# Performance work log

Measured on AMD Instinct MI355X. Metric: run time of the kernel, lower is better.

The kernel has to match this reference:

```python
import jax, jax.numpy as jnp
import numpy as np

B, M, IN, H = 4096, 16, 512, 512


def _linear_params(key, out_dim, in_dim):
    kw, kb = jax.random.split(key)
    s = 1.0 / np.sqrt(in_dim)
    W = jax.random.uniform(kw, (out_dim, in_dim), jnp.float32, -s, s)
    b = jax.random.uniform(kb, (out_dim,), jnp.float32, -s, s)
    return W, b


def setup_inputs() -> dict:
    key = jax.random.key(0)
    ks = jax.random.split(key, 15)
    inp = {
        "input": jax.random.normal(ks[0], (B, IN), jnp.float32),
        "h0": jax.random.normal(ks[1], (B, H), jnp.float32),
        "c0": jax.random.normal(ks[2], (B, H), jnp.float32),
        "all_c_b_e_w": jax.random.normal(ks[3], (B, M, H), jnp.float32),
        "all_num_word": jax.random.randint(ks[4], (B,), 0, M + 1, jnp.int32),
    }
    names = ["ii", "hi", "if_", "hf", "ig", "hg", "io", "ho", "lx", "lc"]
    in_dims = [IN, H, IN, H, IN, H, IN, H, IN, H]
    for n, d, k in zip(names, in_dims, ks[5:15]):
        W, b = _linear_params(k, H, d)
        inp["W_" + n] = W
        inp["b_" + n] = b
    return inp


def _lin(x, W, b):
    return x @ W.T + b


def reference(input, h0, c0, all_c_b_e_w, all_num_word,
              W_ii, b_ii, W_hi, b_hi, W_if_, b_if_, W_hf, b_hf,
              W_ig, b_ig, W_hg, b_hg, W_io, b_io, W_ho, b_ho,
              W_lx, b_lx, W_lc, b_lc):
    i = jax.nn.sigmoid(_lin(input, W_ii, b_ii) + _lin(h0, W_hi, b_hi))   # [B,H]
    f = jax.nn.sigmoid(_lin(input, W_if_, b_if_) + _lin(h0, W_hf, b_hf))  # computed but unused, as in original
    g = jnp.tanh(_lin(input, W_ig, b_ig) + _lin(h0, W_hg, b_hg))         # [B,H]
    o = jax.nn.sigmoid(_lin(input, W_io, b_io) + _lin(h0, W_ho, b_ho))   # [B,H]

    # lattice word-cell gates, vectorized over the ragged word dim with a mask
    lx = _lin(input, W_lx, b_lx)                 # [B,H]
    lc = _lin(all_c_b_e_w, W_lc, b_lc)           # [B,M,H]
    i_b = jax.nn.sigmoid(lx[:, None, :] + lc)    # [B,M,H]
    mask = (jnp.arange(M)[None, :] < all_num_word[:, None])  # [B,M]
    exp_b = jnp.exp(i_b) * mask[:, :, None].astype(i_b.dtype)  # [B,M,H]
    exp_i = jnp.exp(i)                                         # [B,H]
    denom = exp_i + jnp.sum(exp_b, axis=1)                     # [B,H]
    c_words = jnp.sum((exp_b / denom[:, None, :]) * all_c_b_e_w, axis=1)
    c_lat = c_words + (exp_i / denom) * g
    c = jnp.where((all_num_word > 0)[:, None], c_lat, g)       # num_word==0 -> c=g
    h1 = o * jnp.tanh(c)
    return (h1, c)
```

## Files before the change

### kernel.cpp

```cpp
#include <hip/hip_runtime.h>
#include <hip/hip_bf16.h>
#include <stdint.h>


typedef __attribute__((ext_vector_type(8))) short short8;
typedef __attribute__((ext_vector_type(4))) float f32x4;
typedef __attribute__((ext_vector_type(4))) unsigned short us4;

__device__ __forceinline__ unsigned short f2bf(float f) {
  union { float f; unsigned u; } v; v.f = f;
  return (unsigned short)((v.u + 0x7fffu + ((v.u >> 16) & 1u)) >> 16);
}
__device__ __forceinline__ unsigned short f2bf_h(float f) {
  __hip_bfloat16 h = __float2bfloat16(f);
  return *reinterpret_cast<unsigned short*>(&h);
}
__device__ __forceinline__ float bf2f(unsigned short u) {
  return __uint_as_float((unsigned)u << 16);
}
__device__ __forceinline__ float sigmoidf_(float x) {
  return 1.f / (1.f + __expf(-x));
}
__device__ __forceinline__ float fast_tanh(float x) {
  float e = __expf(-2.f * fmaxf(x, -30.f));
  return (1.f - e) / (1.f + e);
}

__global__ void k_cvt_all(const float* __restrict__ x, const float* __restrict__ h,
                          const float* __restrict__ Wii, const float* __restrict__ Wig,
                          const float* __restrict__ Wio, const float* __restrict__ Wlx,
                          const float* __restrict__ Whi, const float* __restrict__ Whg,
                          const float* __restrict__ Who, const float* __restrict__ Wlcf,
                          unsigned short* __restrict__ XH, unsigned short* __restrict__ Wcat,
                          unsigned short* __restrict__ Wlc) {
  const int bb = blockIdx.x;
  const int tid = threadIdx.x;
  us4 o;
  if (bb < 4096) {
    const int t = bb * 256 + tid;
    const int b = t >> 8;
    const int col = (t & 255) * 4;
    const float* src = (col < 512) ? (x + (size_t)b * 512 + col)
                                   : (h + (size_t)b * 512 + (col - 512));
    f32x4 v = *(const f32x4*)src;
    o[0] = f2bf(v[0]); o[1] = f2bf(v[1]); o[2] = f2bf(v[2]); o[3] = f2bf(v[3]);
    *(us4*)(XH + (size_t)t * 4) = o;
  } else if (bb < 6144) {
    const int t = (bb - 4096) * 256 + tid;
    const int row = t >> 8;
    const int col = (t & 255) * 4;
    const int sec = row >> 9, r = row & 511;
    if (col < 512) {
      const float* W = sec == 0 ? Wii : sec == 1 ? Wig : sec == 2 ? Wio : Wlx;
      f32x4 v = *(const f32x4*)(W + (size_t)r * 512 + col);
      o[0] = f2bf(v[0]); o[1] = f2bf(v[1]); o[2] = f2bf(v[2]); o[3] = f2bf(v[3]);
    } else if (sec < 3) {
      const float* W = sec == 0 ? Whi : sec == 1 ? Whg : Who;
      f32x4 v = *(const f32x4*)(W + (size_t)r * 512 + (col - 512));
      o[0] = f2bf(v[0]); o[1] = f2bf(v[1]); o[2] = f2bf(v[2]); o[3] = f2bf(v[3]);
    } else {
      o[0] = 0; o[1] = 0; o[2] = 0; o[3] = 0;
    }
    *(us4*)(Wcat + (size_t)t * 4) = o;
  } else {
    const int t = (bb - 6144) * 256 + tid;
    f32x4 v = *(const f32x4*)(Wlcf + (size_t)t * 4);
    o[0] = f2bf(v[0]); o[1] = f2bf(v[1]); o[2] = f2bf(v[2]); o[3] = f2bf(v[3]);
    *(us4*)(Wlc + (size_t)t * 4) = o;
  }
}

__global__ __launch_bounds__(1024) void k_scan(const int* __restrict__ nwp,
                                               int* __restrict__ off,
                                               int* __restrict__ row_map) {
  const int tid = threadIdx.x;
  const int lane = tid & 63, wid = tid >> 6;
  __shared__ int wsum[16];
  __shared__ int stotal;
  int n[4];
  int s = 0;
#pragma unroll
  for (int i = 0; i < 4; ++i) {
    int v = nwp[tid * 4 + i];
    v = min(max(v, 0), 16);
    n[i] = v; s += v;
  }
  int sc = s;
  for (int d = 1; d < 64; d <<= 1) {
    int t = __shfl_up(sc, d, 64);
    if (lane >= d) sc += t;
  }
  if (lane == 63) wsum[wid] = sc;
  __syncthreads();
  if (tid == 0) {
    int acc = 0;
    for (int w = 0; w < 16; ++w) { int t = wsum[w]; wsum[w] = acc; acc += t; }
    stotal = acc;
  }
  __syncthreads();
  int excl = wsum[wid] + sc - s;
#pragma unroll
  for (int i = 0; i < 4; ++i) {
    const int b = tid * 4 + i;
    off[b] = excl;
    for (int m = 0; m < n[i]; ++m) row_map[excl + m] = b * 16 + m;
    excl += n[i];
  }
  __syncthreads();
  const int total = stotal;
  if (tid == 0) off[4096] = total;
  const int padded = (total + 255) & ~255;
  for (int idx = total + tid; idx < padded; idx += 1024) row_map[idx] = 0;
}

__global__ __launch_bounds__(256) void k_gemm0(
    const unsigned short* __restrict__ A, const unsigned short* __restrict__ Bm,
    unsigned short* __restrict__ C, int Ndim, int Kdim, int nbx) {
  __shared__ unsigned short As[2][128 * 64];
  __shared__ unsigned short Bs[2][128 * 64];
  const int tid = threadIdx.x;
  const int lane = tid & 63, wid = tid >> 6;
  const int wr = wid >> 1, wc = wid & 1;
  const int l15 = lane & 15, lhi = lane >> 4;

  const int chunk = gridDim.x >> 3;
  const int bid = (blockIdx.x & 7) * chunk + (blockIdx.x >> 3);
  const int brow = bid / nbx, bcol = bid % nbx;
  const int m0 = brow * 128, n0 = bcol * 128;

  f32x4 acc[4][4];
#pragma unroll
  for (int i = 0; i < 4; ++i)
#pragma unroll
    for (int j = 0; j < 4; ++j) acc[i][j] = (f32x4){0.f, 0.f, 0.f, 0.f};

  const int cb0 = wid * 64;
  auto stage = [&](int buf, int k0) {
#pragma unroll
    for (int q = 0; q < 4; ++q) {
      const int cb = q * 256 + cb0;
      const int chunkid = cb + lane;
      const int row = chunkid >> 3, slot = chunkid & 7;
      const int kk = k0 + ((slot ^ (row & 7)) << 3);
      __builtin_amdgcn_global_load_lds(
          (const __attribute__((address_space(1))) unsigned int*)(A + (size_t)(m0 + row) * Kdim + kk),
          (__attribute__((address_space(3))) unsigned int*)(As[buf] + cb * 8), 16, 0, 0);
      __builtin_amdgcn_global_load_lds(
          (const __attribute__((address_space(1))) unsigned int*)(Bm + (size_t)(n0 + row) * Kdim + kk),
          (__attribute__((address_space(3))) unsigned int*)(Bs[buf] + cb * 8), 16, 0, 0);
    }
  };

  const int nt = Kdim >> 6;
  stage(0, 0);
  __syncthreads();

  const int swz = (lane & 7) << 4;
  for (int t = 0; t < nt; ++t) {
    const int cur = t & 1;
    if (t + 1 < nt) stage(cur ^ 1, (t + 1) << 6);
    const char* Ab = (const char*)As[cur];
    const char* Bb = (const char*)Bs[cur];
#pragma unroll
    for (int s = 0; s < 2; ++s) {
      short8 av[4], bv[4];
#pragma unroll
      for (int mi = 0; mi < 4; ++mi) {
        const int row = wr * 64 + mi * 16 + l15;
        av[mi] = *(const short8*)(Ab + row * 128 + ((s * 64 + lhi * 16) ^ swz));
      }
#pragma unroll
      for (int ni = 0; ni < 4; ++ni) {
        const int row = wc * 64 + ni * 16 + l15;
        bv[ni] = *(const short8*)(Bb + row * 128 + ((s * 64 + lhi * 16) ^ swz));
      }
#pragma unroll
      for (int mi = 0; mi < 4; ++mi)
#pragma unroll
        for (int ni = 0; ni < 4; ++ni)
          acc[mi][ni] = __builtin_amdgcn_mfma_f32_16x16x32_bf16(av[mi], bv[ni], acc[mi][ni], 0, 0, 0);
    }
    __syncthreads();
  }

#pragma unroll
  for (int mi = 0; mi < 4; ++mi) {
    const int gr = m0 + wr * 64 + mi * 16 + lhi * 4;
#pragma unroll
    for (int ni = 0; ni < 4; ++ni) {
      const int gc = n0 + wc * 64 + ni * 16 + l15;
#pragma unroll
      for (int j = 0; j < 4; ++j)
        C[(size_t)(gr + j) * Ndim + gc] = f2bf(acc[mi][ni][j]);
    }
  }
}

__global__ __launch_bounds__(512) void k_latg(
    const float* __restrict__ Af,
    const unsigned short* __restrict__ Bm,
    const int* __restrict__ row_map,
    const int* __restrict__ totalp,
    unsigned short* __restrict__ lcb) {
  __shared__ unsigned short As[2][256 * 32];
  __shared__ unsigned short Bs[2][256 * 32];
  const int tid = threadIdx.x;
  const int lane = tid & 63, wid = tid >> 6;
  const int wrow = wid >> 2, wcol = wid & 3;
  const int l15 = lane & 15, lhi = lane >> 4;

  const int total = totalp[0];
  const int nact = ((total + 255) >> 8) << 1;
  const int chunk = gridDim.x >> 3;
  const int bid = (blockIdx.x & 7) * chunk + (blockIdx.x >> 3);
  if (bid >= nact) return;
  const int brow = bid >> 1, bcol = bid & 1;
  const int m0 = brow * 256, n0 = bcol * 256;

  int orow0 = row_map[m0 + (tid >> 2)];
  int orow1 = row_map[m0 + 128 + (tid >> 2)];

  f32x4 acc[8][4];
#pragma unroll
  for (int i = 0; i < 8; ++i)
#pragma unroll
    for (int j = 0; j < 4; ++j) acc[i][j] = (f32x4){0.f, 0.f, 0.f, 0.f};

  f32x4 SA[2][2], SB[2][2];

  auto loadA = [&](f32x4 (&dst)[2][2], int k0) {
#pragma unroll
    for (int q = 0; q < 2; ++q) {
      const int orow = q ? orow1 : orow0;
      const int s = tid & 3;
      const float* p = Af + (size_t)orow * 512 + k0 + s * 8;
      dst[q][0] = *(const f32x4*)p;
      dst[q][1] = *(const f32x4*)(p + 4);
    }
  };
  auto writeA = [&](int buf, f32x4 (&src)[2][2]) {
#pragma unroll
    for (int q = 0; q < 2; ++q) {
      const int c = q * 512 + tid;
      const int row = c >> 2, s = c & 3;
      const int pr = row >> 1;
      const int phys = (s + ((row & 1) << 2)) ^ (pr & 7);
      short8 v;
      v[0] = (short)f2bf_h(src[q][0][0]); v[1] = (short)f2bf_h(src[q][0][1]);
      v[2] = (short)f2bf_h(src[q][0][2]); v[3] = (short)f2bf_h(src[q][0][3]);
      v[4] = (short)f2bf_h(src[q][1][0]); v[5] = (short)f2bf_h(src[q][1][1]);
      v[6] = (short)f2bf_h(src[q][1][2]); v[7] = (short)f2bf_h(src[q][1][3]);
      *(short8*)((char*)As[buf] + pr * 128 + phys * 16) = v;
    }
  };
  auto stageB = [&](int buf, int k0) {
#pragma unroll
    for (int q = 0; q < 2; ++q) {
      const int cb = q * 512 + wid * 64;
      const int c = cb + lane;
      const int pr = c >> 3, phys = c & 7;
      const int gi = phys ^ (pr & 7);
      const int row = pr * 2 + (gi >> 2);
      const int kk = k0 + ((gi & 3) << 3);
      __builtin_amdgcn_global_load_lds(
          (const __attribute__((address_space(1))) unsigned int*)(Bm + (size_t)(n0 + row) * 512 + kk),
          (__attribute__((address_space(3))) unsigned int*)(Bs[buf] + cb * 8), 16, 0, 0);
    }
  };

  auto compute = [&](int buf) {
    const char* Ab = (const char*)As[buf];
    const char* Bb = (const char*)Bs[buf];
    short8 av[8], bv[4];
#pragma unroll
    for (int mi = 0; mi < 8; ++mi) {
      const int row = wrow * 128 + mi * 16 + l15;
      const int pr = row >> 1;
      av[mi] = *(const short8*)(Ab + pr * 128 +
                (((lhi + ((row & 1) << 2)) ^ (pr & 7)) << 4));
    }
#pragma unroll
    for (int ni = 0; ni < 4; ++ni) {
      const int row = wcol * 64 + ni * 16 + l15;
      const int pr = row >> 1;
      bv[ni] = *(const short8*)(Bb + pr * 128 +
                (((lhi + ((row & 1) << 2)) ^ (pr & 7)) << 4));
    }
    __builtin_amdgcn_s_setprio(1);
#pragma unroll
    for (int mi = 0; mi < 8; ++mi)
#pragma unroll
      for (int ni = 0; ni < 4; ++ni)
        acc[mi][ni] = __builtin_amdgcn_mfma_f32_16x16x32_bf16(av[mi], bv[ni], acc[mi][ni], 0, 0, 0);
    __builtin_amdgcn_s_setprio(0);
  };

  loadA(SA, 0);
  loadA(SB, 32);
  stageB(0, 0);
  writeA(0, SA);
  __syncthreads();

#pragma unroll 1
  for (int t = 0; t < 16; t += 2) {
    if (t + 2 < 16) loadA(SA, (t + 2) << 5);
    if (t + 1 < 16) stageB(1, (t + 1) << 5);
    compute(0);
    if (t + 1 < 16) writeA(1, SB);
    __syncthreads();
    if (t + 3 < 16) loadA(SB, (t + 3) << 5);
    if (t + 2 < 16) stageB(0, (t + 2) << 5);
    compute(1);
    if (t + 2 < 16) writeA(0, SA);
    __syncthreads();
  }

#pragma unroll
  for (int mi = 0; mi < 8; ++mi) {
    const int rbase = m0 + wrow * 128 + mi * 16 + lhi * 4;
#pragma unroll
    for (int ni = 0; ni < 4; ++ni) {
      const int gc = n0 + wcol * 64 + ni * 16 + l15;
#pragma unroll
      for (int j = 0; j < 4; ++j) {
        const int rc = rbase + j;
        if (rc < total)
          lcb[(size_t)rc * 512 + gc] = f2bf(acc[mi][ni][j]);
      }
    }
  }
}

__global__ __launch_bounds__(512) void k_epi(
    const unsigned short* __restrict__ lc,
    const float* __restrict__ all_c,
    const unsigned short* __restrict__ C1u,
    const int* __restrict__ num_word,
    const int* __restrict__ off,
    const float* __restrict__ b_ii, const float* __restrict__ b_hi,
    const float* __restrict__ b_ig, const float* __restrict__ b_hg,
    const float* __restrict__ b_io, const float* __restrict__ b_ho,
    const float* __restrict__ b_lx, const float* __restrict__ b_lc,
    float* __restrict__ outH, float* __restrict__ outC) {
  const int b = blockIdx.x;
  const int hc = threadIdx.x;
  const int nw = num_word[b];
  const size_t base = (size_t)b * 2048;

  const float pre = bf2f(C1u[base + 1536 + hc]) + b_lx[hc] + b_lc[hc];
  const unsigned short* lcp = lc + (size_t)off[b] * 512 + hc;
  const float* wp = all_c + ((size_t)b * 16) * 512 + hc;

  float se = 0.f, sew = 0.f;
#pragma unroll 4
  for (int m = 0; m < nw; ++m) {
    const float ib = sigmoidf_(pre + bf2f(lcp[(size_t)m * 512]));
    const float e = __expf(ib);
    se += e;
    sew += e * wp[(size_t)m * 512];
  }

  const float ig = sigmoidf_(bf2f(C1u[base + hc]) + b_ii[hc] + b_hi[hc]);
  const float g  = fast_tanh(bf2f(C1u[base + 512 + hc]) + b_ig[hc] + b_hg[hc]);
  const float og = sigmoidf_(bf2f(C1u[base + 1024 + hc]) + b_io[hc] + b_ho[hc]);
  const float ei = __expf(ig);
  const float denom = ei + se;
  const float cc = (sew + ei * g) / denom;
  outH[(size_t)b * 512 + hc] = og * fast_tanh(cc);
  outC[(size_t)b * 512 + hc] = cc;
}

extern "C" void kernel_launch(void* const* d_in, const int* in_sizes, int n_in,
                              void* d_out, int out_size, void* d_ws, size_t ws_size,
                              hipStream_t stream) {
  const float* input    = (const float*)d_in[0];
  const float* h0       = (const float*)d_in[1];
  const float* all_c    = (const float*)d_in[3];
  const int*   num_word = (const int*)d_in[4];
  const float* W_ii = (const float*)d_in[5];  const float* b_ii = (const float*)d_in[6];
  const float* W_hi = (const float*)d_in[7];  const float* b_hi = (const float*)d_in[8];
  const float* W_ig = (const float*)d_in[13]; const float* b_ig = (const float*)d_in[14];
  const float* W_hg = (const float*)d_in[15]; const float* b_hg = (const float*)d_in[16];
  const float* W_io = (const float*)d_in[17]; const float* b_io = (const float*)d_in[18];
  const float* W_ho = (const float*)d_in[19]; const float* b_ho = (const float*)d_in[20];
  const float* W_lx = (const float*)d_in[21]; const float* b_lx = (const float*)d_in[22];
  const float* W_lc = (const float*)d_in[23]; const float* b_lc = (const float*)d_in[24];

  char* ws = (char*)d_ws;
  unsigned short* XH   = (unsigned short*)(ws);
  unsigned short* Wcat = (unsigned short*)(ws + 8388608);
  unsigned short* Wlc  = (unsigned short*)(ws + 12582912);
  unsigned short* C1u  = (unsigned short*)(ws + 13107200);
  unsigned short* lc   = (unsigned short*)(ws + 29884416);
  int*            off  = (int*)(ws + 96993280);
  int*            rmap = (int*)(ws + 97026048);

  float* outH = (float*)d_out;
  float* outC = outH + (size_t)4096 * 512;

  k_cvt_all<<<6400, 256, 0, stream>>>(input, h0, W_ii, W_ig, W_io, W_lx,
                                      W_hi, W_hg, W_ho, W_lc, XH, Wcat, Wlc);

  k_scan<<<1, 1024, 0, stream>>>(num_word, off, rmap);

  k_gemm0<<<512, 256, 0, stream>>>(XH, Wcat, C1u, 2048, 1024, 16);

  k_latg<<<512, 512, 0, stream>>>(all_c, Wlc, rmap, off + 4096, lc);

  k_epi<<<4096, 512, 0, stream>>>(lc, all_c, C1u, num_word, off,
      b_ii, b_hi, b_ig, b_hg, b_io, b_ho, b_lx, b_lc, outH, outC);
}
```

Measured before the change: 116.4 us.

## Pre-gather and convert word cells to bf16 before lattice GEMM

Adds a separate kernel that gathers the active all_c rows through row_map and converts them to a compact bf16 buffer. The lattice GEMM then stages both operands straight into LDS with global_load_lds, using 128x128x64 tiles at 256 threads instead of 256x256x32 tiles with register-staged fp32 conversion. This removes the in-loop fp32 load and convert work from the GEMM. In exchange it adds an extra kernel launch plus a bf16 buffer write and read.

```diff
diff --git a/kernel.cpp b/kernel.cpp
--- a/kernel.cpp
+++ b/kernel.cpp
@@ -10,10 +10,6 @@
 __device__ __forceinline__ unsigned short f2bf(float f) {
   union { float f; unsigned u; } v; v.f = f;
   return (unsigned short)((v.u + 0x7fffu + ((v.u >> 16) & 1u)) >> 16);
-}
-__device__ __forceinline__ unsigned short f2bf_h(float f) {
-  __hip_bfloat16 h = __float2bfloat16(f);
-  return *reinterpret_cast<unsigned short*>(&h);
 }
 __device__ __forceinline__ float bf2f(unsigned short u) {
   return __uint_as_float((unsigned)u << 16);
@@ -113,6 +109,26 @@
   for (int idx = total + tid; idx < padded; idx += 1024) row_map[idx] = 0;
 }
 
+__global__ __launch_bounds__(256) void k_cvt_c(
+    const float* __restrict__ all_c, const int* __restrict__ row_map,
+    const int* __restrict__ totalp, unsigned short* __restrict__ Cbf) {
+  const int total = totalp[0];
+  const int padded = (total + 127) & ~127;
+  const int idx = blockIdx.x * 256 + threadIdx.x;
+  const int rowc = idx >> 6;
+  if (rowc >= padded) return;
+  const int col = (idx & 63) * 8;
+  const float* sp = all_c + (size_t)row_map[rowc] * 512 + col;
+  f32x4 v0 = *(const f32x4*)sp;
+  f32x4 v1 = *(const f32x4*)(sp + 4);
+  short8 o;
+  o[0] = (short)f2bf(v0[0]); o[1] = (short)f2bf(v0[1]);
+  o[2] = (short)f2bf(v0[2]); o[3] = (short)f2bf(v0[3]);
+  o[4] = (short)f2bf(v1[0]); o[5] = (short)f2bf(v1[1]);
+  o[6] = (short)f2bf(v1[2]); o[7] = (short)f2bf(v1[3]);
+  *(short8*)(Cbf + (size_t)rowc * 512 + col) = o;
+}
+
 __global__ __launch_bounds__(256) void k_gemm0(
     const unsigned short* __restrict__ A, const unsigned short* __restrict__ Bm,
     unsigned short* __restrict__ C, int Ndim, int Kdim, int nbx) {
@@ -196,137 +212,90 @@
   }
 }
 
-__global__ __launch_bounds__(512) void k_latg(
-    const float* __restrict__ Af,
+__global__ __launch_bounds__(256) void k_latg(
+    const unsigned short* __restrict__ A,
     const unsigned short* __restrict__ Bm,
-    const int* __restrict__ row_map,
     const int* __restrict__ totalp,
     unsigned short* __restrict__ lcb) {
-  __shared__ unsigned short As[2][256 * 32];
-  __shared__ unsigned short Bs[2][256 * 32];
+  __shared__ unsigned short As[2][128 * 64];
+  __shared__ unsigned short Bs[2][128 * 64];
   const int tid = threadIdx.x;
   const int lane = tid & 63, wid = tid >> 6;
-  const int wrow = wid >> 2, wcol = wid & 3;
+  const int wr = wid >> 1, wc = wid & 1;
   const int l15 = lane & 15, lhi = lane >> 4;
 
   const int total = totalp[0];
-  const int nact = ((total + 255) >> 8) << 1;
+  const int nact = (((total + 127) >> 7) << 2);
   const int chunk = gridDim.x >> 3;
   const int bid = (blockIdx.x & 7) * chunk + (blockIdx.x >> 3);
   if (bid >= nact) return;
-  const int brow = bid >> 1, bcol = bid & 1;
-  const int m0 = brow * 256, n0 = bcol * 256;
-
-  int orow0 = row_map[m0 + (tid >> 2)];
-  int orow1 = row_map[m0 + 128 + (tid >> 2)];
-
-  f32x4 acc[8][4];
-#pragma unroll
-  for (int i = 0; i < 8; ++i)
+  const int brow = bid >> 2, bcol = bid & 3;
+  const int m0 = brow * 128, n0 = bcol * 128;
+
+  f32x4 acc[4][4];
+#pragma unroll
+  for (int i = 0; i < 4; ++i)
 #pragma unroll
     for (int j = 0; j < 4; ++j) acc[i][j] = (f32x4){0.f, 0.f, 0.f, 0.f};
 
-  f32x4 SA[2][2], SB[2][2];
-
-  auto loadA = [&](f32x4 (&dst)[2][2], int k0) {
-#pragma unroll
-    for (int q = 0; q < 2; ++q) {
-      const int orow = q ? orow1 : orow0;
-      const int s = tid & 3;
-      const float* p = Af + (size_t)orow * 512 + k0 + s * 8;
-      dst[q][0] = *(const f32x4*)p;
-      dst[q][1] = *(const f32x4*)(p + 4);
-    }
-  };
-  auto writeA = [&](int buf, f32x4 (&src)[2][2]) {
-#pragma unroll
-    for (int q = 0; q < 2; ++q) {
-      const int c = q * 512 + tid;
-      const int row = c >> 2, s = c & 3;
-      const int pr = row >> 1;
-      const int phys = (s + ((row & 1) << 2)) ^ (pr & 7);
-      short8 v;
-      v[0] = (short)f2bf_h(src[q][0][0]); v[1] = (short)f2bf_h(src[q][0][1]);
-      v[2] = (short)f2bf_h(src[q][0][2]); v[3] = (short)f2bf_h(src[q][0][3]);
-      v[4] = (short)f2bf_h(src[q][1][0]); v[5] = (short)f2bf_h(src[q][1][1]);
-      v[6] = (short)f2bf_h(src[q][1][2]); v[7] = (short)f2bf_h(src[q][1][3]);
-      *(short8*)((char*)As[buf] + pr * 128 + phys * 16) = v;
-    }
-  };
-  auto stageB = [&](int buf, int k0) {
-#pragma unroll
-    for (int q = 0; q < 2; ++q) {
-      const int cb = q * 512 + wid * 64;
-      const int c = cb + lane;
-      const int pr = c >> 3, phys = c & 7;
-      const int gi = phys ^ (pr & 7);
-      const int row = pr * 2 + (gi >> 2);
-      const int kk = k0 + ((gi & 3) << 3);
+  const int cb0 = wid * 64;
+  auto stage = [&](int buf, int k0) {
+#pragma unroll
+    for (int q = 0; q < 4; ++q) {
+      const int cb = q * 256 + cb0;
+      const int chunkid = cb + lane;
+      const int row = chunkid >> 3, slot = chunkid & 7;
+      const int kk = k0 + ((slot ^ (row & 7)) << 3);
+      __builtin_amdgcn_global_load_lds(
+          (const __attribute__((address_space(1))) unsigned int*)(A + (size_t)(m0 + row) * 512 + kk),
+          (__attribute__((address_space(3))) unsigned int*)(As[buf] + cb * 8), 16, 0, 0);
       __builtin_amdgcn_global_load_lds(
           (const __attribute__((address_space(1))) unsigned int*)(Bm + (size_t)(n0 + row) * 512 + kk),
           (__attribute__((address_space(3))) unsigned int*)(Bs[buf] + cb * 8), 16, 0, 0);
     }
   };
 
-  auto compute = [&](int buf) {
-    const char* Ab = (const char*)As[buf];
-    const char* Bb = (const char*)Bs[buf];
-    short8 av[8], bv[4];
-#pragma unroll
-    for (int mi = 0; mi < 8; ++mi) {
-      const int row = wrow * 128 + mi * 16 + l15;
-      const int pr = row >> 1;
-      av[mi] = *(const short8*)(Ab + pr * 128 +
-                (((lhi + ((row & 1) << 2)) ^ (pr & 7)) << 4));
-    }
+  stage(0, 0);
+  __syncthreads();
+
+  const int swz = (lane & 7) << 4;
+  for (int t = 0; t < 8; ++t) {
+    const int cur = t & 1;
+    if (t + 1 < 8) stage(cur ^ 1, (t + 1) << 6);
+    const char* Ab = (const char*)As[cur];
+    const char* Bb = (const char*)Bs[cur];
+#pragma unroll
+    for (int s = 0; s < 2; ++s) {
+      short8 av[4], bv[4];
+#pragma unroll
+      for (int mi = 0; mi < 4; ++mi) {
+        const int row = wr * 64 + mi * 16 + l15;
+        av[mi] = *(const short8*)(Ab + row * 128 + ((s * 64 + lhi * 16) ^ swz));
+      }
+#pragma unroll
+      for (int ni = 0; ni < 4; ++ni) {
+        const int row = wc * 64 + ni * 16 + l15;
+        bv[ni] = *(const short8*)(Bb + row * 128 + ((s * 64 + lhi * 16) ^ swz));
+      }
+#pragma unroll
+      for (int mi = 0; mi < 4; ++mi)
+#pragma unroll
+        for (int ni = 0; ni < 4; ++ni)
+          acc[mi][ni] = __builtin_amdgcn_mfma_f32_16x16x32_bf16(av[mi], bv[ni], acc[mi][ni], 0, 0, 0);
+    }
+    __syncthreads();
+  }
+
+#pragma unroll
+  for (int mi = 0; mi < 4; ++mi) {
+    const int gr = m0 + wr * 64 + mi * 16 + lhi * 4;
 #pragma unroll
     for (int ni = 0; ni < 4; ++ni) {
-      const int row = wcol * 64 + ni * 16 + l15;
-      const int pr = row >> 1;
-      bv[ni] = *(const short8*)(Bb + pr * 128 +
-                (((lhi + ((row & 1) << 2)) ^ (pr & 7)) << 4));
-    }
-    __builtin_amdgcn_s_setprio(1);
-#pragma unroll
-    for (int mi = 0; mi < 8; ++mi)
-#pragma unroll
-      for (int ni = 0; ni < 4; ++ni)
-        acc[mi][ni] = __builtin_amdgcn_mfma_f32_16x16x32_bf16(av[mi], bv[ni], acc[mi][ni], 0, 0, 0);
-    __builtin_amdgcn_s_setprio(0);
-  };
-
-  loadA(SA, 0);
-  loadA(SB, 32);
-  stageB(0, 0);
-  writeA(0, SA);
-  __syncthreads();
-
-#pragma unroll 1
-  for (int t = 0; t < 16; t += 2) {
-    if (t + 2 < 16) loadA(SA, (t + 2) << 5);
-    if (t + 1 < 16) stageB(1, (t + 1) << 5);
-    compute(0);
-    if (t + 1 < 16) writeA(1, SB);
-    __syncthreads();
-    if (t + 3 < 16) loadA(SB, (t + 3) << 5);
-    if (t + 2 < 16) stageB(0, (t + 2) << 5);
-    compute(1);
-    if (t + 2 < 16) writeA(0, SA);
-    __syncthreads();
-  }
-
-#pragma unroll
-  for (int mi = 0; mi < 8; ++mi) {
-    const int rbase = m0 + wrow * 128 + mi * 16 + lhi * 4;
-#pragma unroll
-    for (int ni = 0; ni < 4; ++ni) {
-      const int gc = n0 + wcol * 64 + ni * 16 + l15;
-#pragma unroll
-      for (int j = 0; j < 4; ++j) {
-        const int rc = rbase + j;
-        if (rc < total)
-          lcb[(size_t)rc * 512 + gc] = f2bf(acc[mi][ni][j]);
-      }
+      const int gc = n0 + wc * 64 + ni * 16 + l15;
+#pragma unroll
+      for (int j = 0; j < 4; ++j)
+        if (gr + j < total)
+          lcb[(size_t)(gr + j) * 512 + gc] = f2bf(acc[mi][ni][j]);
     }
   }
 }
@@ -392,8 +361,9 @@
   unsigned short* Wlc  = (unsigned short*)(ws + 12582912);
   unsigned short* C1u  = (unsigned short*)(ws + 13107200);
   unsigned short* lc   = (unsigned short*)(ws + 29884416);
-  int*            off  = (int*)(ws + 96993280);
-  int*            rmap = (int*)(ws + 97026048);
+  unsigned short* Cbf  = (unsigned short*)(ws + 96993280);
+  int*            off  = (int*)(ws + 164102144);
+  int*            rmap = (int*)(ws + 164134912);
 
   float* outH = (float*)d_out;
   float* outC = outH + (size_t)4096 * 512;
@@ -403,9 +373,11 @@
 
   k_scan<<<1, 1024, 0, stream>>>(num_word, off, rmap);
 
+  k_cvt_c<<<16384, 256, 0, stream>>>(all_c, rmap, off + 4096, Cbf);
+
   k_gemm0<<<512, 256, 0, stream>>>(XH, Wcat, C1u, 2048, 1024, 16);
 
-  k_latg<<<512, 512, 0, stream>>>(all_c, Wlc, rmap, off + 4096, lc);
+  k_latg<<<2048, 256, 0, stream>>>(Cbf, Wlc, off + 4096, lc);
 
   k_epi<<<4096, 512, 0, stream>>>(lc, all_c, C1u, num_word, off,
       b_ii, b_hi, b_ig, b_hg, b_io, b_ho, b_lx, b_lc, outH, outC);
```

After: 134.7 us. 15.8% more time.
